# Performance work log

Measured on AMD Instinct MI355X. Metric: run time of the kernel, lower is better.

## Reference

```python
import jax, jax.numpy as jnp
import numpy as np

H, DH = 12, 64
EPS = 1e-6
ROPE_BASE = 100.0

def rms_norm(x, scale=None, eps=EPS):
    xf = x.astype(jnp.float32)
    n = xf * jax.lax.rsqrt(jnp.mean(xf * xf, axis=-1, keepdims=True) + eps)
    if scale is not None:
        n = n * scale.astype(jnp.float32)
    return n.astype(x.dtype)

def rotate_half(x):
    h = x.shape[-1] // 2
    return jnp.concatenate([-x[..., h:], x[..., :h]], axis=-1)

def rope_cos_sin(pos_ids, head_dim, base=ROPE_BASE):
    # pos_ids: [B, N, 2] int -> cos/sin [B, N, head_dim]
    dim = head_dim // 2
    inv = 1.0 / base ** (jnp.arange(0, dim, 2, dtype=jnp.float32) / dim)  # [dim//2]
    cos_l, sin_l = [], []
    for i in range(2):  # x and y coordinate
        pos = pos_ids[:, :, i].astype(jnp.float32)           # [B, N]
        freqs = pos[:, :, None] * inv[None, None, :]          # [B, N, dim//2]
        emb = jnp.concatenate([freqs, freqs], axis=-1)        # [B, N, dim]
        cos_l.append(jnp.cos(emb))
        sin_l.append(jnp.sin(emb))
    return jnp.concatenate(cos_l, axis=-1), jnp.concatenate(sin_l, axis=-1)

def apply_2d_rope(x, cos, sin):
    # x: [B, N, H, Dh]; cos/sin: [B, N, Dh]; split channels evenly between x/y.
    c = x.shape[-1] // 2
    outs = []
    for k in range(2):
        xs = x[..., k * c:(k + 1) * c]
        cc = cos[:, :, None, k * c:(k + 1) * c]
        ss = sin[:, :, None, k * c:(k + 1) * c]
        outs.append(xs * cc + rotate_half(xs) * ss)
    return jnp.concatenate(outs, axis=-1)

def setup_inputs() -> dict:
    key = jax.random.key(0)
    ks = jax.random.split(key, 7)
    B, N, D = 8, 1024, 768
    hidden_states = jax.random.normal(ks[0], (B, N, D), dtype=jnp.float32)
    pixel_position_ids = jax.random.randint(ks[1], (B, N, 2), 0, 32, dtype=jnp.int32)
    s = 0.02
    Wq = jax.random.normal(ks[2], (H * DH, D), dtype=jnp.float32) * s
    Wk = jax.random.normal(ks[3], (H * DH, D), dtype=jnp.float32) * s
    Wv = jax.random.normal(ks[4], (H * DH, D), dtype=jnp.float32) * s
    Wo = jax.random.normal(ks[5], (D, H * DH), dtype=jnp.float32) * s
    q_scale = jnp.ones((DH,), dtype=jnp.float32)
    k_scale = jnp.ones((DH,), dtype=jnp.float32)
    return {"hidden_states": hidden_states, "pixel_position_ids": pixel_position_ids,
            "Wq": Wq, "Wk": Wk, "Wv": Wv, "Wo": Wo,
            "q_scale": q_scale, "k_scale": k_scale}

def reference(hidden_states, pixel_position_ids, Wq, Wk, Wv, Wo, q_scale, k_scale):
    B, N, D = hidden_states.shape
    # QKV projections (clip bounds are +/-inf -> no-op). Weights are [out, in].
    q = (hidden_states @ Wq.T).reshape(B, N, H, DH)
    k = (hidden_states @ Wk.T).reshape(B, N, H, DH)
    v = (hidden_states @ Wv.T).reshape(B, N, H, DH)
    # Per-head RMSNorm (v has no learned scale)
    q = rms_norm(q, q_scale)
    k = rms_norm(k, k_scale)
    v = rms_norm(v, None)
    # 2D RoPE
    cos, sin = rope_cos_sin(pixel_position_ids, DH)
    q = apply_2d_rope(q, cos, sin)
    k = apply_2d_rope(k, cos, sin)
    # Full attention, scaling = 1.0, softmax in fp32
    scores = jnp.einsum('bqhd,bkhd->bhqk', q, k)
    attn = jax.nn.softmax(scores.astype(jnp.float32), axis=-1).astype(q.dtype)
    out = jnp.einsum('bhqk,bkhd->bqhd', attn, v).reshape(B, N, H * DH)
    return out @ Wo.T
```

## Files before the change

### kernel.cpp

```cpp
#include <hip/hip_runtime.h>

typedef _Float16 f16;
typedef __attribute__((ext_vector_type(8))) _Float16 f16x8;
typedef __attribute__((ext_vector_type(4))) _Float16 f16x4;
typedef __attribute__((ext_vector_type(2))) __fp16 h16x2;
typedef __attribute__((ext_vector_type(4))) float f32x4;

#define NH 12
#define DHD 64
#define NB 8
#define NSEQ 1024
#define DMODEL 768
#define BHN (NB*NH)
#define ROWS_PER (BHN*NSEQ)

#define MFMA(a,b,c) __builtin_amdgcn_mfma_f32_16x16x32_f16(a,b,c,0,0,0)

__device__ __forceinline__ void gload16(const void* g, void* l) {
  __builtin_amdgcn_global_load_lds(
      (__attribute__((address_space(1))) void*)(g),
      (__attribute__((address_space(3))) void*)(l), 16, 0, 0);
}

__global__ __launch_bounds__(256) void cast_kernel(const float* __restrict__ in,
                                                   f16* __restrict__ out, int n) {
  int i = (blockIdx.x * blockDim.x + threadIdx.x) * 4;
  if (i < n) {
    float4 v = *(const float4*)(in + i);
    f16x4 o = {(f16)v.x, (f16)v.y, (f16)v.z, (f16)v.w};
    *(f16x4*)(out + i) = o;
  }
}

__global__ __launch_bounds__(256) void cast_w_kernel(const float* __restrict__ Wq,
                                                     const float* __restrict__ Wk,
                                                     const float* __restrict__ Wv,
                                                     const float* __restrict__ Wo,
                                                     f16* __restrict__ Wf,
                                                     f16* __restrict__ Wof,
                                                     float2* __restrict__ rtab, int nw) {
  int i = (blockIdx.x * blockDim.x + threadIdx.x) * 4;
  if (i < 4*nw) {
    int which = i / nw;
    int off = i - which*nw;
    const float* src = (which == 0) ? Wq : (which == 1) ? Wk : (which == 2) ? Wv : Wo;
    f16* dst = (which < 3) ? (Wf + (size_t)which*nw + off) : (Wof + off);
    float4 v = *(const float4*)(src + off);
    f16x4 o = {(f16)v.x, (f16)v.y, (f16)v.z, (f16)v.w};
    *(f16x4*)dst = o;
  }
  if (blockIdx.x == 0) {
    for (int e = threadIdx.x; e < 512; e += 256) {
      int pos = e >> 4, k = e & 15;
      float ang = (float)pos * __expf((float)k * (-4.605170185988091f / 16.0f));
      float sn, cs;
      __sincosf(ang, &sn, &cs);
      rtab[e] = make_float2(cs, sn);
    }
  }
}

template<int MODE>
__global__ __launch_bounds__(256) void gemm_bt(const f16* __restrict__ A,
                                               const f16* __restrict__ B,
                                               float* __restrict__ Cout,
                                               f16* __restrict__ QKout,
                                               f16* __restrict__ Vout,
                                               const int* __restrict__ pos_ids,
                                               const float* __restrict__ q_scale,
                                               const float* __restrict__ k_scale,
                                               const float2* __restrict__ rtab,
                                               int M, int N, int K) {
  constexpr int BN = (MODE == 1) ? 128 : 64;
  constexpr int NJ = BN / 32;
  constexpr int ABUF = 8192;
  constexpr int BBUF = BN*64;
  __shared__ __align__(16) f16 SH[2*ABUF + 2*BBUF];
  const int tid = threadIdx.x;
  const int w = tid >> 6, l = tid & 63;
  const int wr = w >> 1, wc = w & 1;
  const int g = l >> 4, i16 = l & 15;

  int bx, by;
  {
    int id = blockIdx.x;
    const int nbx = (MODE == 1) ? 18 : 12;
    const int chunk = (MODE == 1) ? 144 : 96;
    int idp = (id & 7) * chunk + (id >> 3);
    by = idp / nbx; bx = idp - by * nbx;
  }

  const f32x4 fzero = {0.f, 0.f, 0.f, 0.f};
  f32x4 acc[4][NJ];
#pragma unroll
  for (int i = 0; i < 4; i++)
#pragma unroll
    for (int j = 0; j < NJ; j++) acc[i][j] = fzero;

  const int srow = tid >> 3;
  const int schunk = (tid & 7) ^ (srow & 7);
  const size_t arow = (size_t)(by*128 + srow)*K + schunk*8;
  const size_t brow = (size_t)(bx*BN + srow)*K + schunk*8;

  const int nt = K / 64;
#define STAGE(buf, k0)                                                          \
  {                                                                             \
    char* AlB = (char*)(SH + (buf)*ABUF) + w*1024;                              \
    char* BlB = (char*)(SH + 2*ABUF + (buf)*BBUF) + w*1024;                     \
    _Pragma("unroll")                                                           \
    for (int n = 0; n < 4; ++n)                                                 \
      gload16(A + arow + (size_t)(n*32)*K + (k0), AlB + n*4096);                \
    _Pragma("unroll")                                                           \
    for (int n = 0; n < BN/32; ++n)                                             \
      gload16(B + brow + (size_t)(n*32)*K + (k0), BlB + n*4096);                \
  }

  STAGE(0, 0);
  __syncthreads();
  for (int t = 0; t < nt; ++t) {
    const int buf = t & 1;
    if (t + 1 < nt) STAGE(buf ^ 1, (t + 1)*64);
    const f16* Ac = SH + buf*ABUF;
    const f16* Bc = SH + 2*ABUF + buf*BBUF;
#pragma unroll
    for (int kk = 0; kk < 2; ++kk) {
      f16x8 af[4], bfr[NJ];
#pragma unroll
      for (int i = 0; i < 4; i++)
        af[i] = *(const f16x8*)(Ac + (wr*64 + i*16 + i16)*64 + ((kk*4 + g) ^ (i16 & 7))*8);
#pragma unroll
      for (int j = 0; j < NJ; j++)
        bfr[j] = *(const f16x8*)(Bc + (wc*(BN/2) + j*16 + i16)*64 + ((kk*4 + g) ^ (i16 & 7))*8);
#pragma unroll
      for (int i = 0; i < 4; i++)
#pragma unroll
        for (int j = 0; j < NJ; j++)
          acc[i][j] = MFMA(af[i], bfr[j], acc[i][j]);
    }
    __syncthreads();
  }
#undef STAGE

  const int m0 = by*128 + wr*64;
  const int n0 = bx*BN + wc*(BN/2);
  if constexpr (MODE == 0) {
#pragma unroll
    for (int i = 0; i < 4; i++)
#pragma unroll
      for (int j = 0; j < NJ; j++)
#pragma unroll
        for (int r = 0; r < 4; r++) {
          int m = m0 + i*16 + g*4 + r;
          int n = n0 + j*16 + i16;
          Cout[(size_t)m*N + n] = acc[i][j][r];
        }
  } else {
  if (bx >= 12) {
    const int h0 = (bx - 12)*2;
    const int bb = by >> 3;
    const int ns0 = (by & 7) * 128;
    f16* Lt = SH;
#pragma unroll
    for (int i = 0; i < 4; i++) {
      f32x4 ssv = fzero;
#pragma unroll
      for (int j = 0; j < 4; j++)
#pragma unroll
        for (int r = 0; r < 4; r++) ssv[r] += acc[i][j][r]*acc[i][j][r];
#pragma unroll
      for (int d = 1; d < 16; d <<= 1)
#pragma unroll
        for (int r = 0; r < 4; r++) ssv[r] += __shfl_xor(ssv[r], d);
#pragma unroll
      for (int r = 0; r < 4; r++) {
        float rinv = rsqrtf(ssv[r] * (1.0f/64.0f) + 1e-6f);
        int nsl = wr*64 + i*16 + g*4 + r;
#pragma unroll
        for (int j = 0; j < 4; j++)
          Lt[(wc*64 + j*16 + i16)*136 + nsl] = (f16)(acc[i][j][r]*rinv);
      }
    }
    __syncthreads();
    const int dh = tid >> 1, half = tid & 1;
    f16* dst = Vout + ((size_t)((bb*NH + h0 + (dh >> 6))*64 + (dh & 63)))*1024
               + ns0 + half*64;
    const f16* ls = Lt + dh*136 + half*64;
#pragma unroll
    for (int e = 0; e < 8; ++e)
      *(uint4*)(dst + e*8) = *(const uint4*)(ls + e*8);
  } else {
    const int qkv = n0 / DMODEL;
    const int h = (n0 - qkv*DMODEL) >> 6;
    const float* scp = (qkv == 0) ? q_scale : k_scale;
    float scl[4];
#pragma unroll
    for (int j = 0; j < 4; j++) {
      scl[j] = scp[j*16 + i16];
      if (qkv == 0) scl[j] *= 1.4426950408889634f;
    }
    const float2* rt = rtab + i16;
#pragma unroll
    for (int i = 0; i < 4; i++) {
      f32x4 ssv = fzero;
#pragma unroll
      for (int j = 0; j < 4; j++)
#pragma unroll
        for (int r = 0; r < 4; r++) ssv[r] += acc[i][j][r]*acc[i][j][r];
#pragma unroll
      for (int d = 1; d < 16; d <<= 1)
#pragma unroll
        for (int r = 0; r < 4; r++) ssv[r] += __shfl_xor(ssv[r], d);
#pragma unroll
      for (int r = 0; r < 4; r++) {
        int m = m0 + i*16 + g*4 + r;
        int bb = m >> 10, ns = m & 1023;
        float rinv = rsqrtf(ssv[r] * (1.0f/64.0f) + 1e-6f);
        int2 pp = *(const int2*)(pos_ids + ((size_t)bb*NSEQ + ns)*2);
        float2 t0 = rt[pp.x*16];
        float2 t1 = rt[pp.y*16];
        float x0 = acc[i][0][r]*rinv*scl[0];
        float x1 = acc[i][1][r]*rinv*scl[1];
        float x2 = acc[i][2][r]*rinv*scl[2];
        float x3 = acc[i][3][r]*rinv*scl[3];
        size_t row = ((size_t)qkv*BHN + bb*NH + h)*NSEQ + ns;
        f16* ob = QKout + row*64;
        ob[i16]      = (f16)(x0*t0.x - x1*t0.y);
        ob[16 + i16] = (f16)(x1*t0.x + x0*t0.y);
        ob[32 + i16] = (f16)(x2*t1.x - x3*t1.y);
        ob[48 + i16] = (f16)(x3*t1.x + x2*t1.y);
      }
    }
  }
  }
}

__device__ __forceinline__ int sigma_perm(int p) {
  return (p & 0x20) | ((p & 0xC) << 1) | ((p & 0x10) >> 2) | (p & 3);
}

#define FM3(a,b,c) fmaxf(fmaxf(a,b),c)

__global__ __launch_bounds__(256) void attn_kernel(const f16* __restrict__ QKu,
                                                   const f16* __restrict__ Vtu,
                                                   f16* __restrict__ O) {
  const int bh = blockIdx.y;
  const int q0 = blockIdx.x * 64;
  const int tid = threadIdx.x, w = tid >> 6, l = tid & 63;
  const int g = l >> 4, i16 = l & 15;
  const int g4 = g*4;
  const int sw = i16 & 7;
  const int b = bh / NH, h = bh - b*NH;

  __shared__ __align__(16) f16 Ks[2*64*64];
  __shared__ __align__(16) f16 Vs[2*64*64];

  const f16* qrow = QKu + ((size_t)bh*NSEQ + q0 + w*16 + i16)*64;
  f16x8 q0f = *(const f16x8*)(qrow + g*8);
  f16x8 q1f = *(const f16x8*)(qrow + 32 + g*8);

  const char* Kb  = (const char*)(QKu + (size_t)(BHN + bh)*NSEQ*64);
  const char* Vtb = (const char*)(Vtu + (size_t)bh*64*1024);
  const int prow0 = w*8 + (l >> 3);
  const int cl = (l & 7) ^ (l >> 3);
  const char* Ksrc0 = Kb + sigma_perm(prow0)*128 + cl*16;
  const char* Ksrc1 = Kb + (sigma_perm(prow0) + 32)*128 + cl*16;
  const char* Vsrc0 = Vtb + prow0*2048 + cl*16;
  const char* Vsrc1 = Vtb + (prow0 + 32)*2048 + cl*16;

  const f32x4 fzero = {0.f, 0.f, 0.f, 0.f};
  const f16x8 vones = {(f16)1.f,(f16)1.f,(f16)1.f,(f16)1.f,
                       (f16)1.f,(f16)1.f,(f16)1.f,(f16)1.f};
  float mR = -1e30f;
  f32x4 o[4];
  f32x4 acc_l = fzero;
#pragma unroll
  for (int t = 0; t < 4; t++) o[t] = fzero;

  int cur = 0;
  {
    char* kd = (char*)Ks + w*1024;
    char* vd = (char*)Vs + w*1024;
    gload16(Ksrc0, kd);
    gload16(Ksrc1, kd + 4096);
    gload16(Vsrc0, vd);
    gload16(Vsrc1, vd + 4096);
  }
  __syncthreads();

  for (int t = 0; t < 16; ++t) {
    if (t < 15) {
      char* kd = (char*)Ks + (cur^1)*8192 + w*1024;
      char* vd = (char*)Vs + (cur^1)*8192 + w*1024;
      gload16(Ksrc0 + (t+1)*8192, kd);
      gload16(Ksrc1 + (t+1)*8192, kd + 4096);
      gload16(Vsrc0 + (t+1)*128,  vd);
      gload16(Vsrc1 + (t+1)*128,  vd + 4096);
    }
    const f16* Kc = Ks + cur*4096;
    const f16* Vc = Vs + cur*4096;

    f32x4 s[4] = {fzero, fzero, fzero, fzero};
    __builtin_amdgcn_s_setprio(1);
#pragma unroll
    for (int j = 0; j < 4; ++j) {
      const f16* kr = Kc + (j*16 + i16)*64;
      f16x8 k0 = *(const f16x8*)(kr + (g ^ sw)*8);
      f16x8 k1 = *(const f16x8*)(kr + ((g^4) ^ sw)*8);
      s[j] = MFMA(k0, q0f, s[j]);
      s[j] = MFMA(k1, q1f, s[j]);
    }
    __builtin_amdgcn_s_setprio(0);

    float t0m = FM3(s[0][0], s[0][1], s[0][2]);
    float t1m = FM3(s[0][3], s[1][0], s[1][1]);
    float t2m = FM3(s[1][2], s[1][3], s[2][0]);
    float t3m = FM3(s[2][1], s[2][2], s[2][3]);
    float t4m = FM3(s[3][0], s[3][1], s[3][2]);
    float tm = fmaxf(FM3(FM3(t0m, t1m, t2m), t3m, t4m), s[3][3]);
    tm = fmaxf(tm, __shfl_xor(tm, 16));
    tm = fmaxf(tm, __shfl_xor(tm, 32));
    if (__any(tm > mR + 11.5416f)) {
      float nm = fmaxf(mR, tm);
      float fac = __builtin_amdgcn_exp2f(mR - nm);
      mR = nm;
#pragma unroll
      for (int r = 0; r < 4; ++r) {
        float fr = __shfl(fac, g4 + r);
        o[0][r] *= fr; o[1][r] *= fr; o[2][r] *= fr; o[3][r] *= fr;
        acc_l[r] *= fr;
      }
    }
#pragma unroll
    for (int j = 0; j < 4; ++j)
#pragma unroll
      for (int r = 0; r < 4; ++r) s[j][r] = __builtin_amdgcn_exp2f(s[j][r] - mR);

    union { h16x2 h[4]; f16x8 v; } u0, u1;
    u0.h[0] = __builtin_amdgcn_cvt_pkrtz(s[0][0], s[0][1]);
    u0.h[1] = __builtin_amdgcn_cvt_pkrtz(s[0][2], s[0][3]);
    u0.h[2] = __builtin_amdgcn_cvt_pkrtz(s[1][0], s[1][1]);
    u0.h[3] = __builtin_amdgcn_cvt_pkrtz(s[1][2], s[1][3]);
    u1.h[0] = __builtin_amdgcn_cvt_pkrtz(s[2][0], s[2][1]);
    u1.h[1] = __builtin_amdgcn_cvt_pkrtz(s[2][2], s[2][3]);
    u1.h[2] = __builtin_amdgcn_cvt_pkrtz(s[3][0], s[3][1]);
    u1.h[3] = __builtin_amdgcn_cvt_pkrtz(s[3][2], s[3][3]);
    f16x8 pa0 = u0.v, pa1 = u1.v;

    __builtin_amdgcn_s_setprio(1);
#pragma unroll
    for (int t2 = 0; t2 < 4; ++t2) {
      const f16* vr = Vc + (t2*16 + i16)*64;
      f16x8 bv0 = *(const f16x8*)(vr + (g ^ sw)*8);
      f16x8 bv1 = *(const f16x8*)(vr + ((g^4) ^ sw)*8);
      o[t2] = MFMA(pa0, bv0, o[t2]);
      o[t2] = MFMA(pa1, bv1, o[t2]);
    }
    acc_l = MFMA(pa0, vones, acc_l);
    acc_l = MFMA(pa1, vones, acc_l);
    __builtin_amdgcn_s_setprio(0);

    __syncthreads();
    cur ^= 1;
  }

#pragma unroll
  for (int r = 0; r < 4; ++r) {
    float invl = 1.0f / acc_l[r];
    int q = q0 + w*16 + g4 + r;
    size_t base = ((size_t)(b*NSEQ + q))*DMODEL + h*DHD;
#pragma unroll
    for (int t2 = 0; t2 < 4; ++t2)
      O[base + t2*16 + i16] = (f16)(o[t2][r] * invl);
  }
}

extern "C" void kernel_launch(void* const* d_in, const int* in_sizes, int n_in,
                              void* d_out, int out_size, void* d_ws, size_t ws_size,
                              hipStream_t stream) {
  const float* hs = (const float*)d_in[0];
  const int*   pos = (const int*)d_in[1];
  const float* Wq = (const float*)d_in[2];
  const float* Wk = (const float*)d_in[3];
  const float* Wv = (const float*)d_in[4];
  const float* Wo = (const float*)d_in[5];
  const float* qs = (const float*)d_in[6];
  const float* ks = (const float*)d_in[7];

  const int nhs = 8192*768;
  const int nw  = 768*768;

  char* p = (char*)d_ws;
  f16* Xf   = (f16*)p; p += (size_t)nhs*2;
  f16* Wf   = (f16*)p; p += (size_t)3*nw*2;
  f16* Wof  = (f16*)p; p += (size_t)nw*2;
  f16* QKpk = (f16*)p; p += (size_t)2*ROWS_PER*64*2;
  f16* Vt   = (f16*)p; p += (size_t)ROWS_PER*64*2;
  f16* Ob   = (f16*)p; p += (size_t)nhs*2;
  float2* Rtab = (float2*)p; p += 512*sizeof(float2);

  cast_kernel<<<nhs/1024, 256, 0, stream>>>(hs, Xf, nhs);
  cast_w_kernel<<<(4*nw)/1024, 256, 0, stream>>>(Wq, Wk, Wv, Wo, Wf, Wof, Rtab, nw);

  gemm_bt<1><<<1152, 256, 0, stream>>>(Xf, Wf, nullptr, QKpk, Vt,
                                       pos, qs, ks, Rtab, 8192, 2304, 768);
  attn_kernel<<<dim3(16, 96), 256, 0, stream>>>(QKpk, Vt, Ob);
  gemm_bt<0><<<768, 256, 0, stream>>>(Ob, Wof, (float*)d_out, nullptr, nullptr,
                                      nullptr, nullptr, nullptr, nullptr, 8192, 768, 768);
}
```

Measured before the change: 131.2 us.

## Process two query tiles per attention block and remap grid to XCDs

```diff
diff --git a/kernel.cpp b/kernel.cpp
--- a/kernel.cpp
+++ b/kernel.cpp
@@ -243,8 +243,10 @@
 __global__ __launch_bounds__(256) void attn_kernel(const f16* __restrict__ QKu,
                                                    const f16* __restrict__ Vtu,
                                                    f16* __restrict__ O) {
-  const int bh = blockIdx.y;
-  const int q0 = blockIdx.x * 64;
+  const int id = blockIdx.x;
+  const int xcd = id & 7, idx = id >> 3;
+  const int bh = xcd*12 + (idx >> 3);
+  const int q0 = (idx & 7) * 128;
   const int tid = threadIdx.x, w = tid >> 6, l = tid & 63;
   const int g = l >> 4, i16 = l & 15;
   const int g4 = g*4;
@@ -254,9 +256,12 @@
   __shared__ __align__(16) f16 Ks[2*64*64];
   __shared__ __align__(16) f16 Vs[2*64*64];
 
-  const f16* qrow = QKu + ((size_t)bh*NSEQ + q0 + w*16 + i16)*64;
-  f16x8 q0f = *(const f16x8*)(qrow + g*8);
-  f16x8 q1f = *(const f16x8*)(qrow + 32 + g*8);
+  const f16* qrow0 = QKu + ((size_t)bh*NSEQ + q0 + w*16 + i16)*64;
+  const f16* qrow1 = qrow0 + 64*64;
+  f16x8 qa0 = *(const f16x8*)(qrow0 + g*8);
+  f16x8 qa1 = *(const f16x8*)(qrow0 + 32 + g*8);
+  f16x8 qb0 = *(const f16x8*)(qrow1 + g*8);
+  f16x8 qb1 = *(const f16x8*)(qrow1 + 32 + g*8);
 
   const char* Kb  = (const char*)(QKu + (size_t)(BHN + bh)*NSEQ*64);
   const char* Vtb = (const char*)(Vtu + (size_t)bh*64*1024);
@@ -270,11 +275,11 @@
   const f32x4 fzero = {0.f, 0.f, 0.f, 0.f};
   const f16x8 vones = {(f16)1.f,(f16)1.f,(f16)1.f,(f16)1.f,
                        (f16)1.f,(f16)1.f,(f16)1.f,(f16)1.f};
-  float mR = -1e30f;
-  f32x4 o[4];
-  f32x4 acc_l = fzero;
-#pragma unroll
-  for (int t = 0; t < 4; t++) o[t] = fzero;
+  float mR0 = -1e30f, mR1 = -1e30f;
+  f32x4 o0[4], o1[4];
+  f32x4 acc_l0 = fzero, acc_l1 = fzero;
+#pragma unroll
+  for (int t = 0; t < 4; t++) { o0[t] = fzero; o1[t] = fzero; }
 
   int cur = 0;
   {
@@ -299,52 +304,90 @@
     const f16* Kc = Ks + cur*4096;
     const f16* Vc = Vs + cur*4096;
 
-    f32x4 s[4] = {fzero, fzero, fzero, fzero};
+    f32x4 s0[4] = {fzero, fzero, fzero, fzero};
+    f32x4 s1[4] = {fzero, fzero, fzero, fzero};
     __builtin_amdgcn_s_setprio(1);
 #pragma unroll
     for (int j = 0; j < 4; ++j) {
       const f16* kr = Kc + (j*16 + i16)*64;
       f16x8 k0 = *(const f16x8*)(kr + (g ^ sw)*8);
       f16x8 k1 = *(const f16x8*)(kr + ((g^4) ^ sw)*8);
-      s[j] = MFMA(k0, q0f, s[j]);
-      s[j] = MFMA(k1, q1f, s[j]);
+      s0[j] = MFMA(k0, qa0, s0[j]);
+      s0[j] = MFMA(k1, qa1, s0[j]);
+      s1[j] = MFMA(k0, qb0, s1[j]);
+      s1[j] = MFMA(k1, qb1, s1[j]);
     }
     __builtin_amdgcn_s_setprio(0);
 
-    float t0m = FM3(s[0][0], s[0][1], s[0][2]);
-    float t1m = FM3(s[0][3], s[1][0], s[1][1]);
-    float t2m = FM3(s[1][2], s[1][3], s[2][0]);
-    float t3m = FM3(s[2][1], s[2][2], s[2][3]);
-    float t4m = FM3(s[3][0], s[3][1], s[3][2]);
-    float tm = fmaxf(FM3(FM3(t0m, t1m, t2m), t3m, t4m), s[3][3]);
-    tm = fmaxf(tm, __shfl_xor(tm, 16));
-    tm = fmaxf(tm, __shfl_xor(tm, 32));
-    if (__any(tm > mR + 11.5416f)) {
-      float nm = fmaxf(mR, tm);
-      float fac = __builtin_amdgcn_exp2f(mR - nm);
-      mR = nm;
-#pragma unroll
-      for (int r = 0; r < 4; ++r) {
-        float fr = __shfl(fac, g4 + r);
-        o[0][r] *= fr; o[1][r] *= fr; o[2][r] *= fr; o[3][r] *= fr;
-        acc_l[r] *= fr;
+    {
+      float t0m = FM3(s0[0][0], s0[0][1], s0[0][2]);
+      float t1m = FM3(s0[0][3], s0[1][0], s0[1][1]);
+      float t2m = FM3(s0[1][2], s0[1][3], s0[2][0]);
+      float t3m = FM3(s0[2][1], s0[2][2], s0[2][3]);
+      float t4m = FM3(s0[3][0], s0[3][1], s0[3][2]);
+      float tm = fmaxf(FM3(FM3(t0m, t1m, t2m), t3m, t4m), s0[3][3]);
+      tm = fmaxf(tm, __shfl_xor(tm, 16));
+      tm = fmaxf(tm, __shfl_xor(tm, 32));
+      if (__any(tm > mR0 + 11.5416f)) {
+        float nm = fmaxf(mR0, tm);
+        float fac = __builtin_amdgcn_exp2f(mR0 - nm);
+        mR0 = nm;
+#pragma unroll
+        for (int r = 0; r < 4; ++r) {
+          float fr = __shfl(fac, g4 + r);
+          o0[0][r] *= fr; o0[1][r] *= fr; o0[2][r] *= fr; o0[3][r] *= fr;
+          acc_l0[r] *= fr;
+        }
       }
-    }
-#pragma unroll
-    for (int j = 0; j < 4; ++j)
-#pragma unroll
-      for (int r = 0; r < 4; ++r) s[j][r] = __builtin_amdgcn_exp2f(s[j][r] - mR);
-
-    union { h16x2 h[4]; f16x8 v; } u0, u1;
-    u0.h[0] = __builtin_amdgcn_cvt_pkrtz(s[0][0], s[0][1]);
-    u0.h[1] = __builtin_amdgcn_cvt_pkrtz(s[0][2], s[0][3]);
-    u0.h[2] = __builtin_amdgcn_cvt_pkrtz(s[1][0], s[1][1]);
-    u0.h[3] = __builtin_amdgcn_cvt_pkrtz(s[1][2], s[1][3]);
-    u1.h[0] = __builtin_amdgcn_cvt_pkrtz(s[2][0], s[2][1]);
-    u1.h[1] = __builtin_amdgcn_cvt_pkrtz(s[2][2], s[2][3]);
-    u1.h[2] = __builtin_amdgcn_cvt_pkrtz(s[3][0], s[3][1]);
-    u1.h[3] = __builtin_amdgcn_cvt_pkrtz(s[3][2], s[3][3]);
-    f16x8 pa0 = u0.v, pa1 = u1.v;
+#pragma unroll
+      for (int j = 0; j < 4; ++j)
+#pragma unroll
+        for (int r = 0; r < 4; ++r) s0[j][r] = __builtin_amdgcn_exp2f(s0[j][r] - mR0);
+    }
+    {
+      float t0m = FM3(s1[0][0], s1[0][1], s1[0][2]);
+      float t1m = FM3(s1[0][3], s1[1][0], s1[1][1]);
+      float t2m = FM3(s1[1][2], s1[1][3], s1[2][0]);
+      float t3m = FM3(s1[2][1], s1[2][2], s1[2][3]);
+      float t4m = FM3(s1[3][0], s1[3][1], s1[3][2]);
+      float tm = fmaxf(FM3(FM3(t0m, t1m, t2m), t3m, t4m), s1[3][3]);
+      tm = fmaxf(tm, __shfl_xor(tm, 16));
+      tm = fmaxf(tm, __shfl_xor(tm, 32));
+      if (__any(tm > mR1 + 11.5416f)) {
+        float nm = fmaxf(mR1, tm);
+        float fac = __builtin_amdgcn_exp2f(mR1 - nm);
+        mR1 = nm;
+#pragma unroll
+        for (int r = 0; r < 4; ++r) {
+          float fr = __shfl(fac, g4 + r);
+          o1[0][r] *= fr; o1[1][r] *= fr; o1[2][r] *= fr; o1[3][r] *= fr;
+          acc_l1[r] *= fr;
+        }
+      }
+#pragma unroll
+      for (int j = 0; j < 4; ++j)
+#pragma unroll
+        for (int r = 0; r < 4; ++r) s1[j][r] = __builtin_amdgcn_exp2f(s1[j][r] - mR1);
+    }
+
+    union { h16x2 h[4]; f16x8 v; } ua0, ua1, ub0, ub1;
+    ua0.h[0] = __builtin_amdgcn_cvt_pkrtz(s0[0][0], s0[0][1]);
+    ua0.h[1] = __builtin_amdgcn_cvt_pkrtz(s0[0][2], s0[0][3]);
+    ua0.h[2] = __builtin_amdgcn_cvt_pkrtz(s0[1][0], s0[1][1]);
+    ua0.h[3] = __builtin_amdgcn_cvt_pkrtz(s0[1][2], s0[1][3]);
+    ua1.h[0] = __builtin_amdgcn_cvt_pkrtz(s0[2][0], s0[2][1]);
+    ua1.h[1] = __builtin_amdgcn_cvt_pkrtz(s0[2][2], s0[2][3]);
+    ua1.h[2] = __builtin_amdgcn_cvt_pkrtz(s0[3][0], s0[3][1]);
+    ua1.h[3] = __builtin_amdgcn_cvt_pkrtz(s0[3][2], s0[3][3]);
+    ub0.h[0] = __builtin_amdgcn_cvt_pkrtz(s1[0][0], s1[0][1]);
+    ub0.h[1] = __builtin_amdgcn_cvt_pkrtz(s1[0][2], s1[0][3]);
+    ub0.h[2] = __builtin_amdgcn_cvt_pkrtz(s1[1][0], s1[1][1]);
+    ub0.h[3] = __builtin_amdgcn_cvt_pkrtz(s1[1][2], s1[1][3]);
+    ub1.h[0] = __builtin_amdgcn_cvt_pkrtz(s1[2][0], s1[2][1]);
+    ub1.h[1] = __builtin_amdgcn_cvt_pkrtz(s1[2][2], s1[2][3]);
+    ub1.h[2] = __builtin_amdgcn_cvt_pkrtz(s1[3][0], s1[3][1]);
+    ub1.h[3] = __builtin_amdgcn_cvt_pkrtz(s1[3][2], s1[3][3]);
+    f16x8 pa0 = ua0.v, pa1 = ua1.v, pb0 = ub0.v, pb1 = ub1.v;
 
     __builtin_amdgcn_s_setprio(1);
 #pragma unroll
@@ -352,11 +395,15 @@
       const f16* vr = Vc + (t2*16 + i16)*64;
       f16x8 bv0 = *(const f16x8*)(vr + (g ^ sw)*8);
       f16x8 bv1 = *(const f16x8*)(vr + ((g^4) ^ sw)*8);
-      o[t2] = MFMA(pa0, bv0, o[t2]);
-      o[t2] = MFMA(pa1, bv1, o[t2]);
-    }
-    acc_l = MFMA(pa0, vones, acc_l);
-    acc_l = MFMA(pa1, vones, acc_l);
+      o0[t2] = MFMA(pa0, bv0, o0[t2]);
+      o0[t2] = MFMA(pa1, bv1, o0[t2]);
+      o1[t2] = MFMA(pb0, bv0, o1[t2]);
+      o1[t2] = MFMA(pb1, bv1, o1[t2]);
+    }
+    acc_l0 = MFMA(pa0, vones, acc_l0);
+    acc_l0 = MFMA(pa1, vones, acc_l0);
+    acc_l1 = MFMA(pb0, vones, acc_l1);
+    acc_l1 = MFMA(pb1, vones, acc_l1);
     __builtin_amdgcn_s_setprio(0);
 
     __syncthreads();
@@ -365,12 +412,16 @@
 
 #pragma unroll
   for (int r = 0; r < 4; ++r) {
-    float invl = 1.0f / acc_l[r];
+    float invl0 = 1.0f / acc_l0[r];
+    float invl1 = 1.0f / acc_l1[r];
     int q = q0 + w*16 + g4 + r;
-    size_t base = ((size_t)(b*NSEQ + q))*DMODEL + h*DHD;
-#pragma unroll
-    for (int t2 = 0; t2 < 4; ++t2)
-      O[base + t2*16 + i16] = (f16)(o[t2][r] * invl);
+    size_t base0 = ((size_t)(b*NSEQ + q))*DMODEL + h*DHD;
+    size_t base1 = ((size_t)(b*NSEQ + q + 64))*DMODEL + h*DHD;
+#pragma unroll
+    for (int t2 = 0; t2 < 4; ++t2) {
+      O[base0 + t2*16 + i16] = (f16)(o0[t2][r] * invl0);
+      O[base1 + t2*16 + i16] = (f16)(o1[t2][r] * invl1);
+    }
   }
 }
 
@@ -403,7 +454,7 @@
 
   gemm_bt<1><<<1152, 256, 0, stream>>>(Xf, Wf, nullptr, QKpk, Vt,
                                        pos, qs, ks, Rtab, 8192, 2304, 768);
-  attn_kernel<<<dim3(16, 96), 256, 0, stream>>>(QKpk, Vt, Ob);
+  attn_kernel<<<768, 256, 0, stream>>>(QKpk, Vt, Ob);
   gemm_bt<0><<<768, 256, 0, stream>>>(Ob, Wof, (float*)d_out, nullptr, nullptr,
                                       nullptr, nullptr, nullptr, nullptr, 8192, 768, 768);
 }
```

New measurement: 136.0 us. 1.04x slower.
